# Performance work log

Measured on AMD Instinct MI355X. Metric: run time of the kernel, lower is better.

## Reference

```python
import jax, jax.numpy as jnp
import numpy as np

D_MODEL = 256
D_HIDDEN = 1024
B, S = 4, 32768


def setup_inputs() -> dict:
    key = jax.random.key(0)
    k_x, k_m, k_w1, k_b1, k_w2, k_b2 = jax.random.split(key, 6)
    x = jax.random.normal(k_x, (B, S, D_MODEL), dtype=jnp.float32)
    # graph_dependency: binary connectivity mask [d_hidden, d_model]
    mask = jax.random.randint(k_m, (D_HIDDEN, D_MODEL), 0, 2, dtype=jnp.int32)
    lim1 = 1.0 / np.sqrt(D_MODEL)
    lim2 = 1.0 / np.sqrt(D_HIDDEN)
    w1 = jax.random.uniform(k_w1, (D_HIDDEN, D_MODEL), jnp.float32, -lim1, lim1)
    b1 = jax.random.uniform(k_b1, (D_HIDDEN,), jnp.float32, -lim1, lim1)
    # reserve=True: maps d_hidden -> d_model with transposed mask
    w2 = jax.random.uniform(k_w2, (D_MODEL, D_HIDDEN), jnp.float32, -lim2, lim2)
    b2 = jax.random.uniform(k_b2, (D_MODEL,), jnp.float32, -lim2, lim2)
    return {"x": x, "w1": w1, "b1": b1, "w2": w2, "b2": b2, "mask": mask}


def reference(x, w1, b1, w2, b2, mask):
    m = mask.astype(x.dtype)                      # [H, D]
    # fc1: graph-masked linear d_model -> d_hidden
    h = jnp.einsum('bsd,hd->bsh', x, w1 * m) + b1  # [B, S, H]
    h = jax.nn.relu(h)
    # fc2 (reserve): graph-masked linear d_hidden -> d_model, transposed mask
    y = jnp.einsum('bsh,dh->bsd', h, w2 * m.T) + b2  # [B, S, D]
    return y
```

## Files before the change

### kernel.cpp

```cpp
#include <hip/hip_runtime.h>


#define D_MODEL 256
#define D_HID   1024
#define MT      64
#define CHUNK   32
#define NCHUNK  (D_HID / CHUNK)
#define CHUNK_ELEMS 8192

typedef __attribute__((ext_vector_type(8))) short short8;
typedef __attribute__((ext_vector_type(4))) float v4f;

__device__ __forceinline__ unsigned short f2bf(float f) {
  union { float f; unsigned int u; } v; v.f = f;
  unsigned int u = v.u;
  return (unsigned short)((u + 0x7FFFu + ((u >> 16) & 1u)) >> 16);
}

__device__ __forceinline__ void async16(void* lds, const void* g) {
  __builtin_amdgcn_global_load_lds(
      (const __attribute__((address_space(1))) unsigned int*)g,
      (__attribute__((address_space(3))) unsigned int*)lds,
      16, 0, 0);
}

__global__ __launch_bounds__(256) void prep_weights(
    const float* __restrict__ w1, const float* __restrict__ w2,
    const int* __restrict__ mask,
    unsigned short* __restrict__ W1p, unsigned short* __restrict__ W2p)
{
  int t = blockIdx.x * 256 + threadIdx.x;
  if (t < 32768) {
    int c    = t >> 10;
    int kk   = (t >> 7) & 7;
    int nf   = (t >> 6) & 1;
    int lane = t & 63;
    int h = c * 32 + nf * 16 + (lane & 15);
    int k = kk * 32 + (lane >> 4) * 8;
    const float* wp = w1 + h * 256 + k;
    const int*   mp = mask + h * 256 + k;
    short8 v;
    #pragma unroll
    for (int j = 0; j < 8; ++j) v[j] = (short)(mp[j] ? f2bf(wp[j]) : 0);
    *(short8*)(W1p + (size_t)t * 8) = v;
  } else {
    int s    = t - 32768;
    int c    = s >> 10;
    int nf2  = (s >> 6) & 15;
    int lane = s & 63;
    int n = nf2 * 16 + (lane & 15);
    int h = c * 32 + (lane >> 4) * 8;
    const float* wp = w2 + n * 1024 + h;
    short8 v;
    #pragma unroll
    for (int j = 0; j < 8; ++j)
      v[j] = (short)(mask[(h + j) * 256 + n] ? f2bf(wp[j]) : 0);
    *(short8*)(W2p + (size_t)s * 8) = v;
  }
}

__global__ __launch_bounds__(256, 3) void ffd_fused(
    const float* __restrict__ X, const float* __restrict__ b1,
    const float* __restrict__ b2,
    const unsigned short* __restrict__ W1p, const unsigned short* __restrict__ W2p,
    float* __restrict__ Y)
{
  __shared__ unsigned short sW1[CHUNK_ELEMS];
  __shared__ unsigned short sW2[CHUNK_ELEMS];
  __shared__ unsigned short sHc[4][16 * 48];

  const int tid  = threadIdx.x;
  const int lane = tid & 63;
  const int w    = tid >> 6;
  const int l16  = lane & 15;
  const int q    = lane >> 4;

  const long rowBase = (long)blockIdx.x * MT + w * 16 + l16;

  short8 xf[8];
  const float* xrow = X + rowBase * D_MODEL;
  #pragma unroll
  for (int kk = 0; kk < 8; ++kk) {
    const float4 f0 = *(const float4*)(xrow + kk * 32 + q * 8);
    const float4 f1 = *(const float4*)(xrow + kk * 32 + q * 8 + 4);
    short8 v;
    v[0] = (short)f2bf(f0.x); v[1] = (short)f2bf(f0.y);
    v[2] = (short)f2bf(f0.z); v[3] = (short)f2bf(f0.w);
    v[4] = (short)f2bf(f1.x); v[5] = (short)f2bf(f1.y);
    v[6] = (short)f2bf(f1.z); v[7] = (short)f2bf(f1.w);
    xf[kk] = v;
  }

  v4f acc[16];
  #pragma unroll
  for (int i = 0; i < 16; ++i) acc[i] = (v4f){0.f, 0.f, 0.f, 0.f};

  unsigned short* sHw = sHc[w];

  for (int c = 0; c < NCHUNK; ++c) {
    __syncthreads();
    {
      const unsigned short* g1 = W1p + (size_t)c * CHUNK_ELEMS + tid * 8;
      const unsigned short* g2 = W2p + (size_t)c * CHUNK_ELEMS + tid * 8;
      #pragma unroll
      for (int i = 0; i < 4; ++i) {
        async16(&sW1[i * 2048 + tid * 8], g1 + i * 2048);
        async16(&sW2[i * 2048 + tid * 8], g2 + i * 2048);
      }
    }
    const float bb0 = b1[c * 32 + l16];
    const float bb1 = b1[c * 32 + 16 + l16];
    __syncthreads();

    v4f h0 = {0.f, 0.f, 0.f, 0.f}, h1 = {0.f, 0.f, 0.f, 0.f};
    #pragma unroll
    for (int kk = 0; kk < 8; ++kk) {
      short8 bf0 = *(const short8*)&sW1[(kk * 2 + 0) * 512 + lane * 8];
      short8 bf1 = *(const short8*)&sW1[(kk * 2 + 1) * 512 + lane * 8];
      h0 = __builtin_amdgcn_mfma_f32_16x16x32_bf16(xf[kk], bf0, h0, 0, 0, 0);
      h1 = __builtin_amdgcn_mfma_f32_16x16x32_bf16(xf[kk], bf1, h1, 0, 0, 0);
    }

    #pragma unroll
    for (int r = 0; r < 4; ++r) {
      float v0 = h0[r] + bb0; v0 = v0 > 0.f ? v0 : 0.f;
      float v1 = h1[r] + bb1; v1 = v1 > 0.f ? v1 : 0.f;
      int row = q * 4 + r;
      sHw[row * 48 + l16]      = f2bf(v0);
      sHw[row * 48 + 16 + l16] = f2bf(v1);
    }
    __threadfence_block();

    short8 af = *(const short8*)&sHw[l16 * 48 + q * 8];
    #pragma unroll
    for (int nf2 = 0; nf2 < 16; ++nf2) {
      short8 bf2 = *(const short8*)&sW2[nf2 * 512 + lane * 8];
      acc[nf2] = __builtin_amdgcn_mfma_f32_16x16x32_bf16(af, bf2, acc[nf2], 0, 0, 0);
    }
  }

  const long orow = (long)blockIdx.x * MT + w * 16;
  #pragma unroll
  for (int nf2 = 0; nf2 < 16; ++nf2) {
    int col = nf2 * 16 + l16;
    float bias = b2[col];
    #pragma unroll
    for (int r = 0; r < 4; ++r) {
      long row = orow + q * 4 + r;
      Y[row * D_MODEL + col] = acc[nf2][r] + bias;
    }
  }
}

extern "C" void kernel_launch(void* const* d_in, const int* in_sizes, int n_in,
                              void* d_out, int out_size, void* d_ws, size_t ws_size,
                              hipStream_t stream) {
  const float* x    = (const float*)d_in[0];
  const float* w1   = (const float*)d_in[1];
  const float* b1   = (const float*)d_in[2];
  const float* w2   = (const float*)d_in[3];
  const float* b2   = (const float*)d_in[4];
  const int*   mask = (const int*)d_in[5];

  unsigned short* W1p = (unsigned short*)d_ws;
  unsigned short* W2p = W1p + (size_t)D_HID * D_MODEL;
  float* Y = (float*)d_out;

  prep_weights<<<256, 256, 0, stream>>>(w1, w2, mask, W1p, W2p);
  ffd_fused<<<131072 / MT, 256, 0, stream>>>(x, b1, b2, W1p, W2p, Y);
}
```

Measured before the change: 180.8 us.

## Switch to 32x32x16 MFMA with 128-row tiles and swizzled hidden staging

Each wave now handles 32 rows instead of 16, so the block tile grows to 128 rows. The 16x16x32 MFMAs are replaced with 32x32x16 bf16 MFMAs, and both weight pre-packing layouts are changed to match the new fragment shapes. The per-wave hidden activation buffer uses an XOR swizzle to reduce LDS bank conflicts. The aim is to halve weight LDS traffic per row and the number of chunk loads per row. In exchange, register pressure rises and occupancy drops from 3 to 2 blocks per CU.

```diff
diff --git a/kernel.cpp b/kernel.cpp
--- a/kernel.cpp
+++ b/kernel.cpp
@@ -3,13 +3,12 @@
 
 #define D_MODEL 256
 #define D_HID   1024
-#define MT      64
-#define CHUNK   32
-#define NCHUNK  (D_HID / CHUNK)
+#define MT      128
+#define NCHUNK  32
 #define CHUNK_ELEMS 8192
 
 typedef __attribute__((ext_vector_type(8))) short short8;
-typedef __attribute__((ext_vector_type(4))) float v4f;
+typedef __attribute__((ext_vector_type(16))) float f32x16;
 
 __device__ __forceinline__ unsigned short f2bf(float f) {
   union { float f; unsigned int u; } v; v.f = f;
@@ -32,11 +31,10 @@
   int t = blockIdx.x * 256 + threadIdx.x;
   if (t < 32768) {
     int c    = t >> 10;
-    int kk   = (t >> 7) & 7;
-    int nf   = (t >> 6) & 1;
+    int kf   = (t >> 6) & 15;
     int lane = t & 63;
-    int h = c * 32 + nf * 16 + (lane & 15);
-    int k = kk * 32 + (lane >> 4) * 8;
+    int h = c * 32 + (lane & 31);
+    int k = kf * 16 + (lane >> 5) * 8;
     const float* wp = w1 + h * 256 + k;
     const int*   mp = mask + h * 256 + k;
     short8 v;
@@ -46,20 +44,20 @@
   } else {
     int s    = t - 32768;
     int c    = s >> 10;
-    int nf2  = (s >> 6) & 15;
+    int cf   = (s >> 7) & 7;
+    int kf2  = (s >> 6) & 1;
     int lane = s & 63;
-    int n = nf2 * 16 + (lane & 15);
-    int h = c * 32 + (lane >> 4) * 8;
-    const float* wp = w2 + n * 1024 + h;
+    int n = cf * 32 + (lane & 31);
+    int h = c * 32 + kf2 * 16 + (lane >> 5) * 8;
     short8 v;
     #pragma unroll
     for (int j = 0; j < 8; ++j)
-      v[j] = (short)(mask[(h + j) * 256 + n] ? f2bf(wp[j]) : 0);
+      v[j] = (short)(mask[(h + j) * 256 + n] ? f2bf(w2[n * 1024 + h + j]) : 0);
     *(short8*)(W2p + (size_t)s * 8) = v;
   }
 }
 
-__global__ __launch_bounds__(256, 3) void ffd_fused(
+__global__ __launch_bounds__(256, 2) void ffd_fused(
     const float* __restrict__ X, const float* __restrict__ b1,
     const float* __restrict__ b2,
     const unsigned short* __restrict__ W1p, const unsigned short* __restrict__ W2p,
@@ -67,35 +65,39 @@
 {
   __shared__ unsigned short sW1[CHUNK_ELEMS];
   __shared__ unsigned short sW2[CHUNK_ELEMS];
-  __shared__ unsigned short sHc[4][16 * 48];
+  __shared__ unsigned short sHc[4][1024];
 
   const int tid  = threadIdx.x;
   const int lane = tid & 63;
   const int w    = tid >> 6;
-  const int l16  = lane & 15;
-  const int q    = lane >> 4;
+  const int l32  = lane & 31;
+  const int q2   = lane >> 5;
 
-  const long rowBase = (long)blockIdx.x * MT + w * 16 + l16;
+  const long rowBase = (long)blockIdx.x * MT + w * 32;
 
-  short8 xf[8];
-  const float* xrow = X + rowBase * D_MODEL;
+  short8 xf[16];
+  const float* xrow = X + (rowBase + l32) * D_MODEL;
   #pragma unroll
-  for (int kk = 0; kk < 8; ++kk) {
-    const float4 f0 = *(const float4*)(xrow + kk * 32 + q * 8);
-    const float4 f1 = *(const float4*)(xrow + kk * 32 + q * 8 + 4);
+  for (int kf = 0; kf < 16; ++kf) {
+    const float4 f0 = *(const float4*)(xrow + kf * 16 + q2 * 8);
+    const float4 f1 = *(const float4*)(xrow + kf * 16 + q2 * 8 + 4);
     short8 v;
     v[0] = (short)f2bf(f0.x); v[1] = (short)f2bf(f0.y);
     v[2] = (short)f2bf(f0.z); v[3] = (short)f2bf(f0.w);
     v[4] = (short)f2bf(f1.x); v[5] = (short)f2bf(f1.y);
     v[6] = (short)f2bf(f1.z); v[7] = (short)f2bf(f1.w);
-    xf[kk] = v;
+    xf[kf] = v;
   }
 
-  v4f acc[16];
+  f32x16 acc[8];
   #pragma unroll
-  for (int i = 0; i < 16; ++i) acc[i] = (v4f){0.f, 0.f, 0.f, 0.f};
+  for (int i = 0; i < 8; ++i) {
+    #pragma unroll
+    for (int j = 0; j < 16; ++j) acc[i][j] = 0.f;
+  }
 
   unsigned short* sHw = sHc[w];
+  const int xorw = (l32 & 6) << 2;
 
   for (int c = 0; c < NCHUNK; ++c) {
     __syncthreads();
@@ -108,46 +110,46 @@
         async16(&sW2[i * 2048 + tid * 8], g2 + i * 2048);
       }
     }
-    const float bb0 = b1[c * 32 + l16];
-    const float bb1 = b1[c * 32 + 16 + l16];
+    const float bb = b1[c * 32 + l32];
     __syncthreads();
 
-    v4f h0 = {0.f, 0.f, 0.f, 0.f}, h1 = {0.f, 0.f, 0.f, 0.f};
+    f32x16 hh;
     #pragma unroll
-    for (int kk = 0; kk < 8; ++kk) {
-      short8 bf0 = *(const short8*)&sW1[(kk * 2 + 0) * 512 + lane * 8];
-      short8 bf1 = *(const short8*)&sW1[(kk * 2 + 1) * 512 + lane * 8];
-      h0 = __builtin_amdgcn_mfma_f32_16x16x32_bf16(xf[kk], bf0, h0, 0, 0, 0);
-      h1 = __builtin_amdgcn_mfma_f32_16x16x32_bf16(xf[kk], bf1, h1, 0, 0, 0);
+    for (int j = 0; j < 16; ++j) hh[j] = 0.f;
+    #pragma unroll
+    for (int kf = 0; kf < 16; ++kf) {
+      short8 bf = *(const short8*)&sW1[kf * 512 + lane * 8];
+      hh = __builtin_amdgcn_mfma_f32_32x32x16_bf16(xf[kf], bf, hh, 0, 0, 0);
     }
 
     #pragma unroll
-    for (int r = 0; r < 4; ++r) {
-      float v0 = h0[r] + bb0; v0 = v0 > 0.f ? v0 : 0.f;
-      float v1 = h1[r] + bb1; v1 = v1 > 0.f ? v1 : 0.f;
-      int row = q * 4 + r;
-      sHw[row * 48 + l16]      = f2bf(v0);
-      sHw[row * 48 + 16 + l16] = f2bf(v1);
+    for (int r = 0; r < 16; ++r) {
+      int rr = (r & 3) + 8 * (r >> 2) + 4 * q2;
+      float v = hh[r] + bb;
+      v = v > 0.f ? v : 0.f;
+      sHw[(rr * 32 + l32) ^ ((rr & 6) << 2)] = f2bf(v);
     }
     __threadfence_block();
 
-    short8 af = *(const short8*)&sHw[l16 * 48 + q * 8];
     #pragma unroll
-    for (int nf2 = 0; nf2 < 16; ++nf2) {
-      short8 bf2 = *(const short8*)&sW2[nf2 * 512 + lane * 8];
-      acc[nf2] = __builtin_amdgcn_mfma_f32_16x16x32_bf16(af, bf2, acc[nf2], 0, 0, 0);
+    for (int kf2 = 0; kf2 < 2; ++kf2) {
+      short8 af = *(const short8*)&sHw[(l32 * 32 + kf2 * 16 + q2 * 8) ^ xorw];
+      #pragma unroll
+      for (int cf = 0; cf < 8; ++cf) {
+        short8 bf2 = *(const short8*)&sW2[(cf * 2 + kf2) * 512 + lane * 8];
+        acc[cf] = __builtin_amdgcn_mfma_f32_32x32x16_bf16(af, bf2, acc[cf], 0, 0, 0);
+      }
     }
   }
 
-  const long orow = (long)blockIdx.x * MT + w * 16;
   #pragma unroll
-  for (int nf2 = 0; nf2 < 16; ++nf2) {
-    int col = nf2 * 16 + l16;
+  for (int cf = 0; cf < 8; ++cf) {
+    int col = cf * 32 + l32;
     float bias = b2[col];
     #pragma unroll
-    for (int r = 0; r < 4; ++r) {
-      long row = orow + q * 4 + r;
-      Y[row * D_MODEL + col] = acc[nf2][r] + bias;
+    for (int r = 0; r < 16; ++r) {
+      long row = rowBase + (r & 3) + 8 * (r >> 2) + 4 * q2;
+      Y[row * D_MODEL + col] = acc[cf][r] + bias;
     }
   }
 }
```

Result: faster. 167.4 us (-7.4%).
